# Performance work log

Hardware: AMD Instinct MI355X
Metric: run time of the kernel (lower is better)

Reference implementation:

```python
import jax, jax.numpy as jnp
import numpy as np

PAD_IND = 3
SOS_IND = 0
NSTEPS = 25
H = 256   # hidden_size
D = 256   # input_size (embedding dim)
L = 3     # lstm_layers


def _lstm_cell(x, h, c, Wih, Whh, bih, bhh):
    # torch LSTM gate order: i, f, g, o
    g = x @ Wih.T + bih + h @ Whh.T + bhh
    i, f, gg, o = jnp.split(g, 4, axis=-1)
    c2 = jax.nn.sigmoid(f) * c + jax.nn.sigmoid(i) * jnp.tanh(gg)
    h2 = jax.nn.sigmoid(o) * jnp.tanh(c2)
    return h2, c2


def setup_inputs() -> dict:
    key = jax.random.key(0)
    ks = jax.random.split(key, 24)
    B, T = 64, 256
    Vin, C = 32000, 32000
    s = 1.0 / np.sqrt(H)

    def u(k, shape):
        return jax.random.uniform(k, shape, jnp.float32, -s, s)

    return dict(
        x=jax.random.randint(ks[0], (B, T), 0, Vin),
        target_val=jax.random.randint(ks[1], (B, NSTEPS), 0, C),
        enc_embed=jax.random.normal(ks[2], (Vin, D), jnp.float32),
        enc_Wih=u(ks[3], (L, 4 * H, D)),
        enc_Whh=u(ks[4], (L, 4 * H, H)),
        enc_bih=u(ks[5], (L, 4 * H)),
        enc_bhh=u(ks[6], (L, 4 * H)),
        Wq=u(ks[7], (H, H)), bq=u(ks[8], (H,)),
        Wk=u(ks[9], (H, H)), bk=u(ks[10], (H,)),
        Wv=u(ks[11], (H, H)), bv=u(ks[12], (H,)),
        Wo=u(ks[13], (H, H)), bo=u(ks[14], (H,)),
        dec_embed=jax.random.normal(ks[15], (C, D), jnp.float32),
        dec_Wih0=u(ks[16], (4 * H, 2 * H)),            # decoder layer 0 input is [emb; ctx] = 2H
        dec_Wih_rest=u(ks[17], (L - 1, 4 * H, H)),
        dec_Whh=u(ks[18], (L, 4 * H, H)),
        dec_bih=u(ks[19], (L, 4 * H)),
        dec_bhh=u(ks[20], (L, 4 * H)),
        dec_W=u(ks[21], (C, H)),
        dec_b=u(ks[22], (C,)),
    )


def reference(x, target_val, enc_embed, enc_Wih, enc_Whh, enc_bih, enc_bhh,
              Wq, bq, Wk, bk, Wv, bv, Wo, bo,
              dec_embed, dec_Wih0, dec_Wih_rest, dec_Whh, dec_bih, dec_bhh,
              dec_W, dec_b):
    B, T = x.shape
    lengths = (x != PAD_IND).sum(axis=1)            # [B], emulates pack_padded_sequence
    emb = enc_embed[x]                              # [B,T,D]
    valid = (jnp.arange(T)[:, None] < lengths[None, :])[..., None]  # [T,B,1]
    h0 = jnp.zeros((L, B, H), emb.dtype)
    c0 = jnp.zeros((L, B, H), emb.dtype)

    def enc_step(carry, inp):
        h, c = carry
        xt, v = inp
        hs, cs = [], []
        z = xt
        for l in range(L):
            hl, cl = _lstm_cell(z, h[l], c[l], enc_Wih[l], enc_Whh[l], enc_bih[l], enc_bhh[l])
            hl = jnp.where(v, hl, h[l])             # freeze state past sequence length
            cl = jnp.where(v, cl, c[l])
            hs.append(hl); cs.append(cl)
            z = hl
        h = jnp.stack(hs); c = jnp.stack(cs)
        return (h, c), jnp.where(v, h[-1], 0.0)     # pad_packed pads with zeros

    (enc_h, enc_c), outs = jax.lax.scan(enc_step, (h0, c0), (jnp.swapaxes(emb, 0, 1), valid))
    enc_hiddens = jnp.swapaxes(outs, 0, 1)          # [B,T,H]

    # attention key/value projections are loop-invariant -> hoist out of decode loop
    kp = enc_hiddens @ Wk.T + bk                    # [B,T,H]
    vp = enc_hiddens @ Wv.T + bv                    # [B,T,H]
    scale = 1.0 / jnp.sqrt(jnp.asarray(H, emb.dtype))
    dec_Wih = [dec_Wih0, dec_Wih_rest[0], dec_Wih_rest[1]]
    tok0 = jnp.full((B,), SOS_IND, jnp.int32)

    def dec_step(carry, _):
        h, c, tok = carry
        e = dec_embed[tok]                          # [B,D]
        q = h.sum(axis=0) @ Wq.T + bq               # prev_state[0].sum(axis=0) -> [B,H]
        scores = jnp.einsum('bh,bth->bt', q, kp) * scale
        attn = jax.nn.softmax(scores, axis=-1)
        ctx = jnp.einsum('bt,bth->bh', attn, vp) @ Wo.T + bo
        z = jnp.concatenate([e, ctx], axis=-1)      # [B,2H]
        hs, cs = [], []
        for l in range(L):
            hl, cl = _lstm_cell(z, h[l], c[l], dec_Wih[l], dec_Whh[l], dec_bih[l], dec_bhh[l])
            hs.append(hl); cs.append(cl)
            z = hl
        h = jnp.stack(hs); c = jnp.stack(cs)
        logits = z @ dec_W.T + dec_b                # [B,C]
        tok = jnp.argmax(logits, axis=-1).astype(jnp.int32)  # greedy feedback (TF ratio = 0)
        return (h, c, tok), logits

    _, logits = jax.lax.scan(dec_step, (enc_h, enc_c, tok0), None, length=NSTEPS)  # [25,B,C]
    return jnp.swapaxes(logits, 0, 1)[:, :, None, :]  # [B,25,1,C] like the torch module
```

## Files before the change

kernel.cpp:

```cpp
#include <hip/hip_runtime.h>
#include <math.h>

#define TT    256
#define NB    64
#define HH    256
#define NSTEP 25
#define NCLS  32000
#define PADI  3

__device__ __align__(16) float g_hring[3][2][NB][HH];
__device__ __align__(16) float g_enchid[TT][NB][HH];
__device__ __align__(16) float g_kp[NB][TT][HH];
__device__ __align__(16) float g_vp[NB][TT][HH];
__device__ __align__(16) float g_cfin[3][NB][HH];
__device__ __align__(16) float g_hdec[2][3][NB][HH];
__device__ __align__(16) float g_z0[NB][512];
__device__ float    g_wmax[256][NB];
__device__ int      g_wmaxi[256][NB];
__device__ int      g_len[NB];
__device__ unsigned g_flags[256];

__global__ void k_zero_flags(){ g_flags[threadIdx.x] = 0u; }

__device__ __forceinline__ float sigf(float v){ return 1.0f / (1.0f + expf(-v)); }

#define SCOPE_AG __HIP_MEMORY_SCOPE_AGENT
typedef unsigned long long u64;
__device__ __forceinline__ float2 ld2(const float* p){
  u64 v = __hip_atomic_load((const u64*)p, __ATOMIC_RELAXED, SCOPE_AG);
  float2 r; __builtin_memcpy(&r, &v, 8); return r;
}
__device__ __forceinline__ void st2(float* p, float2 f){
  u64 v; __builtin_memcpy(&v, &f, 8);
  __hip_atomic_store((u64*)p, v, __ATOMIC_RELAXED, SCOPE_AG);
}
__device__ __forceinline__ float ldc(const float* p){ return __hip_atomic_load(p, __ATOMIC_RELAXED, SCOPE_AG); }
__device__ __forceinline__ void  stc(float* p, float v){ __hip_atomic_store(p, v, __ATOMIC_RELAXED, SCOPE_AG); }
__device__ __forceinline__ int   ldi(const int* p){ return __hip_atomic_load(p, __ATOMIC_RELAXED, SCOPE_AG); }
__device__ __forceinline__ void  sti(int* p, int v){ __hip_atomic_store(p, v, __ATOMIC_RELAXED, SCOPE_AG); }
__device__ __forceinline__ unsigned ldu(const unsigned* p){ return __hip_atomic_load(p, __ATOMIC_RELAXED, SCOPE_AG); }
__device__ __forceinline__ void  stu(unsigned* p, unsigned v){ __hip_atomic_store(p, v, __ATOMIC_RELAXED, SCOPE_AG); }

#define DOT4(a_, x_, w_) (a_) += (x_).x*(w_).x + (x_).y*(w_).y + (x_).z*(w_).z + (x_).w*(w_).w

#define WENC(cb,g,jj,u) (((((cb)*12+(g))*8+(jj))*36)+(u))

__device__ __forceinline__ void gbar(int w, unsigned target){
  asm volatile("s_waitcnt vmcnt(0)" ::: "memory");
  __syncthreads();
  if (threadIdx.x == 0) stu(&g_flags[w], target);
  if (threadIdx.x < 64){
    const int i4 = threadIdx.x * 4;
    for (;;){
      unsigned a0 = ldu(&g_flags[i4+0]);
      unsigned a1 = ldu(&g_flags[i4+1]);
      unsigned a2 = ldu(&g_flags[i4+2]);
      unsigned a3 = ldu(&g_flags[i4+3]);
      if (__all((a0>=target) && (a1>=target) && (a2>=target) && (a3>=target))) break;
      __builtin_amdgcn_s_sleep(1);
    }
  }
  __syncthreads();
}

template<int NCB, int BASE>
__device__ __forceinline__ void dec_gates(const float* sw, const float* i0, const float* i1,
                                          const float* i2, int j, float out4[4]){
  float a0=0.f, a1=0.f, a2=0.f, a3=0.f;
  const float* ips[3] = { i0, i1, i2 };
  #pragma unroll
  for (int cb = 0; cb < NCB; ++cb){
    float2 xin[16];
    #pragma unroll
    for (int u = 0; u < 16; ++u) xin[u] = ld2(ips[cb] + u*16 + 2*j);
    #pragma unroll
    for (int u2 = 0; u2 < 8; ++u2){
      float2 pa = xin[2*u2], pb = xin[2*u2+1];
      const float* wb = &sw[BASE + (((cb*4+0)*8+j)*36) + u2*4];
      float4 w0 = *(const float4*)(wb);
      float4 w1 = *(const float4*)(wb + 288);
      float4 w2 = *(const float4*)(wb + 576);
      float4 w3 = *(const float4*)(wb + 864);
      a0 += pa.x*w0.x + pa.y*w0.y + pb.x*w0.z + pb.y*w0.w;
      a1 += pa.x*w1.x + pa.y*w1.y + pb.x*w1.z + pb.y*w1.w;
      a2 += pa.x*w2.x + pa.y*w2.y + pb.x*w2.z + pb.y*w2.w;
      a3 += pa.x*w3.x + pa.y*w3.y + pb.x*w3.z + pb.y*w3.w;
    }
  }
  #pragma unroll
  for (int m = 1; m < 8; m <<= 1){
    a0 += __shfl_xor(a0, m); a1 += __shfl_xor(a1, m);
    a2 += __shfl_xor(a2, m); a3 += __shfl_xor(a3, m);
  }
  out4[0]=a0; out4[1]=a1; out4[2]=a2; out4[3]=a3;
}

__global__ void __launch_bounds__(512, 1)
k_main(const int*   __restrict__ p_x,
       const float* __restrict__ p_eemb,
       const float* __restrict__ p_eWih,  const float* __restrict__ p_eWhh,
       const float* __restrict__ p_ebih,  const float* __restrict__ p_ebhh,
       const float* __restrict__ p_Wq, const float* __restrict__ p_bq,
       const float* __restrict__ p_Wk, const float* __restrict__ p_bk,
       const float* __restrict__ p_Wv, const float* __restrict__ p_bv,
       const float* __restrict__ p_Wo, const float* __restrict__ p_bo,
       const float* __restrict__ p_demb,
       const float* __restrict__ p_dWih0, const float* __restrict__ p_dWihR,
       const float* __restrict__ p_dWhh,
       const float* __restrict__ p_dbih,  const float* __restrict__ p_dbhh,
       const float* __restrict__ p_dW,    const float* __restrict__ p_db,
       float* __restrict__ p_out)
{
  __shared__ __align__(16) float s_w[8064];
  __shared__ __align__(16) float s_h2[NB*HH];
  __shared__ float s_benc[12];
  __shared__ float s_bdec[12];
  __shared__ __align__(16) float s_hs[256];
  __shared__ __align__(16) float s_q[256];
  __shared__ __align__(16) float s_sc[256];
  __shared__ __align__(16) float s_at[256];
  __shared__ __align__(16) float s_ctx[256];
  __shared__ float s_rv[8];  __shared__ int s_ri[8];
  __shared__ float s_rv2[8][16]; __shared__ int s_ri2[8][16];

  const int w   = blockIdx.x;
  const int tid = threadIdx.x;
  const int b   = tid >> 3;
  const int j   = tid & 7;
  unsigned bar  = 0;

  const int lay0 = (w < 255) ? (w / 85) : 0;
  const int h0   = (w < 255) ? ((w - lay0*85) * 3) : 0;

  for (int fi = tid; fi < 6144; fi += 512){
    int g = fi >> 9, k = fi & 511;
    int e = g >> 2, gt = g & 3;
    int l   = (w < 255) ? lay0 : e;
    int hh2 = (w < 255) ? (h0 + e) : 255;
    int row = gt*256 + hh2;
    float v = (k < 256) ? p_eWih[((size_t)l*1024 + row)*256 + k]
                        : p_eWhh[((size_t)l*1024 + row)*256 + (k - 256)];
    int cb = k >> 8, kk = k & 255;
    s_w[WENC(cb, g, (kk & 15) >> 1, ((kk >> 4) << 1) | (kk & 1))] = v;
  }
  if (tid < 12){
    int e = tid >> 2, gt = tid & 3;
    int l   = (w < 255) ? lay0 : e;
    int hh2 = (w < 255) ? (h0 + e) : 255;
    int row = gt*256 + hh2;
    s_benc[tid] = p_ebih[l*1024 + row] + p_ebhh[l*1024 + row];
  }
  if (w < 64){
    int cnt = 0;
    if (tid < 256) cnt = (p_x[w*TT + tid] != PADI) ? 1 : 0;
    #pragma unroll
    for (int m = 1; m < 64; m <<= 1) cnt += __shfl_xor(cnt, m);
    if ((tid & 63) == 0) s_ri[tid >> 6] = cnt;
    __syncthreads();
    if (tid == 0){ int t2 = 0; for (int q2 = 0; q2 < 8; ++q2) t2 += s_ri[q2]; sti(&g_len[w], t2); }
  }
  if (tid < 192){
    int fi = w*192 + tid;
    int l = fi >> 14, rem = fi & 16383;
    stc(&g_hring[l][1][rem >> 8][rem & 255], 0.f);
  }
  gbar(w, ++bar);

  const int len_b = ldi(&g_len[b]);

  float c_reg[3] = {0.f,0.f,0.f};
  float h_reg[3] = {0.f,0.f,0.f};

  for (int sdiag = 0; sdiag < TT + 2; ++sdiag){
    float acc[12];
    #pragma unroll
    for (int g = 0; g < 12; ++g) acc[g] = 0.f;

    if (w < 255){
      const int t = sdiag - lay0;
      if (t >= 0 && t < TT){
        float2 x2[16], h2[16];
        if (lay0 == 0){
          const float* xs = p_eemb + (size_t)p_x[b*TT + t]*HH;
          #pragma unroll
          for (int u = 0; u < 16; ++u) x2[u] = *(const float2*)(xs + u*16 + 2*j);
        } else {
          const float* xs = &g_hring[lay0-1][t & 1][b][0];
          #pragma unroll
          for (int u = 0; u < 16; ++u) x2[u] = ld2(xs + u*16 + 2*j);
        }
        {
          const float* hsv = &g_hring[lay0][(t & 1) ^ 1][b][0];
          #pragma unroll
          for (int u = 0; u < 16; ++u) h2[u] = ld2(hsv + u*16 + 2*j);
        }
        #pragma unroll
        for (int u2 = 0; u2 < 8; ++u2){
          float2 xa = x2[2*u2], xb = x2[2*u2+1];
          float2 ha = h2[2*u2], hb = h2[2*u2+1];
          #pragma unroll
          for (int g = 0; g < 12; ++g){
            float4 wx = *(const float4*)&s_w[WENC(0, g, j, u2*4)];
            float4 wh = *(const float4*)&s_w[WENC(1, g, j, u2*4)];
            acc[g] += xa.x*wx.x + xa.y*wx.y + xb.x*wx.z + xb.y*wx.w
                    + ha.x*wh.x + ha.y*wh.y + hb.x*wh.z + hb.y*wh.w;
          }
        }
      }
    } else {
      #pragma unroll
      for (int e = 0; e < 3; ++e){
        const int t = sdiag - e;
        if (t >= 0 && t < TT){
          float2 x2[16], h2[16];
          if (e == 0){
            const float* xs = p_eemb + (size_t)p_x[b*TT + t]*HH;
            #pragma unroll
            for (int u = 0; u < 16; ++u) x2[u] = *(const float2*)(xs + u*16 + 2*j);
          } else {
            const float* xs = &g_hring[e-1][t & 1][b][0];
            #pragma unroll
            for (int u = 0; u < 16; ++u) x2[u] = ld2(xs + u*16 + 2*j);
          }
          {
            const float* hsv = &g_hring[e][(t & 1) ^ 1][b][0];
            #pragma unroll
            for (int u = 0; u < 16; ++u) h2[u] = ld2(hsv + u*16 + 2*j);
          }
          #pragma unroll
          for (int u2 = 0; u2 < 8; ++u2){
            float2 xa = x2[2*u2], xb = x2[2*u2+1];
            float2 ha = h2[2*u2], hb = h2[2*u2+1];
            #pragma unroll
            for (int g2 = 0; g2 < 4; ++g2){
              float4 wx = *(const float4*)&s_w[WENC(0, e*4+g2, j, u2*4)];
              float4 wh = *(const float4*)&s_w[WENC(1, e*4+g2, j, u2*4)];
              acc[e*4+g2] += xa.x*wx.x + xa.y*wx.y + xb.x*wx.z + xb.y*wx.w
                           + ha.x*wh.x + ha.y*wh.y + hb.x*wh.z + hb.y*wh.w;
            }
          }
        }
      }
    }

    #pragma unroll
    for (int g = 0; g < 12; ++g){
      float v = acc[g];
      v += __shfl_xor(v, 1); v += __shfl_xor(v, 2); v += __shfl_xor(v, 4);
      acc[g] = v;
    }

    if (j == 0){
      #pragma unroll
      for (int e = 0; e < 3; ++e){
        const int lay = (w < 255) ? lay0 : e;
        const int hh2 = (w < 255) ? (h0 + e) : 255;
        const int t = sdiag - lay;
        if (t >= 0 && t < TT){
          float iv = acc[e*4+0] + s_benc[e*4+0];
          float fv = acc[e*4+1] + s_benc[e*4+1];
          float gv = acc[e*4+2] + s_benc[e*4+2];
          float ov = acc[e*4+3] + s_benc[e*4+3];
          float c2 = sigf(fv)*c_reg[e] + sigf(iv)*tanhf(gv);
          float h2v = sigf(ov)*tanhf(c2);
          bool valid = (t < len_b);
          if (valid){ c_reg[e] = c2; h_reg[e] = h2v; }
          stc(&g_hring[lay][t & 1][b][hh2], h_reg[e]);
          if (lay == 2) stc(&g_enchid[t][b][hh2], valid ? h_reg[e] : 0.f);
        }
      }
    }
    gbar(w, ++bar);
  }

  if (j == 0){
    #pragma unroll
    for (int e = 0; e < 3; ++e){
      const int lay = (w < 255) ? lay0 : e;
      const int hh2 = (w < 255) ? (h0 + e) : 255;
      stc(&g_cfin[lay][b][hh2], c_reg[e]);
    }
  }
  gbar(w, ++bar);

  {
    const int b2 = w >> 2, t0 = (w & 3) * 64;
    const int n1 = tid & 127, rq = tid >> 7;
    for (int p = 0; p < 4; ++p){
      const int n = p*128 + n1;
      const float* wrow = (n < 256) ? (p_Wk + (size_t)n*HH) : (p_Wv + (size_t)(n-256)*HH);
      const float bias  = (n < 256) ? p_bk[n] : p_bv[n-256];
      const float4* wr4 = (const float4*)wrow;
      const float* hb = &g_enchid[t0 + rq*16][b2][0];
      const float4* hr[16];
      #pragma unroll
      for (int r = 0; r < 16; ++r) hr[r] = (const float4*)(hb + (size_t)r*NB*HH);
      float a16[16];
      #pragma unroll
      for (int r = 0; r < 16; ++r) a16[r] = 0.f;
      for (int k4 = 0; k4 < 64; ++k4){
        float4 wv = wr4[k4];
        #pragma unroll
        for (int r = 0; r < 16; ++r){ float4 h4 = hr[r][k4]; DOT4(a16[r], h4, wv); }
      }
      float* orow = (n < 256) ? &g_kp[b2][t0 + rq*16][n] : &g_vp[b2][t0 + rq*16][n-256];
      #pragma unroll
      for (int r = 0; r < 16; ++r) stc(orow + (size_t)r*HH, a16[r] + bias);
    }
  }

  for (int fi = tid; fi < 3072; fi += 512){
    int g = fi / 768, k = fi % 768; int row = g*256 + w;
    float v = (k < 512) ? p_dWih0[(size_t)row*512 + k]
                        : p_dWhh[(size_t)row*HH + (k - 512)];
    int cb = k >> 8, kk = k & 255;
    s_w[(((cb*4 + g)*8 + ((kk & 15) >> 1))*36) + (((kk >> 4) << 1) | (kk & 1))] = v;
  }
  for (int fi = tid; fi < 2048; fi += 512){
    int g = fi / 512, k = fi % 512; int row = g*256 + w;
    float v = (k < 256) ? p_dWihR[(size_t)row*HH + k]
                        : p_dWhh[(size_t)(1024 + row)*HH + (k - 256)];
    int cb = k >> 8, kk = k & 255;
    s_w[3456 + (((cb*4 + g)*8 + ((kk & 15) >> 1))*36) + (((kk >> 4) << 1) | (kk & 1))] = v;
  }
  for (int fi = tid; fi < 2048; fi += 512){
    int g = fi / 512, k = fi % 512; int row = g*256 + w;
    float v = (k < 256) ? p_dWihR[(size_t)(1024 + row)*HH + k]
                        : p_dWhh[(size_t)(2048 + row)*HH + (k - 256)];
    int cb = k >> 8, kk = k & 255;
    s_w[5760 + (((cb*4 + g)*8 + ((kk & 15) >> 1))*36) + (((kk >> 4) << 1) | (kk & 1))] = v;
  }
  if (tid < 12){
    int l = tid >> 2, g = tid & 3; int row = g*256 + w;
    s_bdec[tid] = p_dbih[l*1024 + row] + p_dbhh[l*1024 + row];
  }
  gbar(w, ++bar);

  if (tid < 192){
    int fi = w*192 + tid;
    int l = fi >> 14, rem = fi & 16383;
    stc(&g_hdec[0][l][rem >> 8][rem & 255], ldc(&g_hring[l][1][rem >> 8][rem & 255]));
  }
  float c_d0 = 0.f, c_d1 = 0.f, c_d2 = 0.f;
  if (j == 0){
    c_d0 = ldc(&g_cfin[0][b][w]); c_d1 = ldc(&g_cfin[1][b][w]); c_d2 = ldc(&g_cfin[2][b][w]);
  }
  gbar(w, ++bar);

  for (int st = 0; st < NSTEP; ++st){
    const int slot = st & 1, nxt = slot ^ 1;

    if (w < 64){
      const int bA = w;
      int tok = 0;
      if (st > 0){
        float v = -1e38f; int idx = 0;
        if (tid < 256){ v = ldc(&g_wmax[tid][bA]); idx = ldi(&g_wmaxi[tid][bA]); }
        #pragma unroll
        for (int m = 1; m < 64; m <<= 1){
          float ov = __shfl_xor(v, m); int oi = __shfl_xor(idx, m);
          if (ov > v || (ov == v && oi < idx)){ v = ov; idx = oi; }
        }
        if ((tid & 63) == 0){ s_rv[tid >> 6] = v; s_ri[tid >> 6] = idx; }
        __syncthreads();
        if (tid == 0){
          float bv2 = s_rv[0]; int bi2 = s_ri[0];
          for (int q2 = 1; q2 < 8; ++q2){
            float ov = s_rv[q2]; int oi = s_ri[q2];
            if (ov > bv2 || (ov == bv2 && oi < bi2)){ bv2 = ov; bi2 = oi; }
          }
          s_ri[0] = bi2;
        }
        __syncthreads();
        tok = s_ri[0];
      }
      if (tid < 256)
        s_hs[tid] = ldc(&g_hdec[slot][0][bA][tid]) + ldc(&g_hdec[slot][1][bA][tid])
                  + ldc(&g_hdec[slot][2][bA][tid]);
      __syncthreads();
      if (tid < 256){
        float a = p_bq[tid];
        const float4* wr = (const float4*)(p_Wq + (size_t)tid*HH);
        #pragma unroll 8
        for (int k4 = 0; k4 < 64; ++k4){
          float4 wv = wr[k4]; float4 h4 = *(const float4*)&s_hs[k4*4]; DOT4(a, h4, wv);
        }
        s_q[tid] = a;
      }
      __syncthreads();
      if (tid < 256){
        float a = 0.f;
        const float4* kr = (const float4*)&g_kp[bA][tid][0];
        #pragma unroll 8
        for (int k4 = 0; k4 < 64; ++k4){
          float4 kv = kr[k4]; float4 q4 = *(const float4*)&s_q[k4*4]; DOT4(a, q4, kv);
        }
        s_sc[tid] = a * 0.0625f;
      }
      __syncthreads();
      {
        float sv = (tid < 256) ? s_sc[tid] : -1e38f;
        float m2 = sv;
        #pragma unroll
        for (int m = 1; m < 64; m <<= 1) m2 = fmaxf(m2, __shfl_xor(m2, m));
        if ((tid & 63) == 0) s_rv[tid >> 6] = m2;
        __syncthreads();
        if (tid == 0){ float mm = s_rv[0]; for (int q2 = 1; q2 < 8; ++q2) mm = fmaxf(mm, s_rv[q2]); s_rv[0] = mm; }
        __syncthreads();
        const float mx = s_rv[0];
        float ev = (tid < 256) ? expf(sv - mx) : 0.f;
        float ss = ev;
        #pragma unroll
        for (int m = 1; m < 64; m <<= 1) ss += __shfl_xor(ss, m);
        __syncthreads();
        if ((tid & 63) == 0) s_rv[tid >> 6] = ss;
        __syncthreads();
        if (tid == 0){ float t2 = 0.f; for (int q2 = 0; q2 < 8; ++q2) t2 += s_rv[q2]; s_rv[0] = t2; }
        __syncthreads();
        if (tid < 256) s_at[tid] = ev / s_rv[0];
      }
      __syncthreads();
      if (tid < 256){
        float a = 0.f;
        const float* vb = &g_vp[bA][0][tid];
        #pragma unroll 4
        for (int t4 = 0; t4 < 64; ++t4){
          float4 a4 = *(const float4*)&s_at[t4*4];
          a += a4.x*vb[(size_t)(t4*4+0)*HH] + a4.y*vb[(size_t)(t4*4+1)*HH]
             + a4.z*vb[(size_t)(t4*4+2)*HH] + a4.w*vb[(size_t)(t4*4+3)*HH];
        }
        s_ctx[tid] = a;
      }
      __syncthreads();
      if (tid < 256){
        float a = p_bo[tid];
        const float4* wr = (const float4*)(p_Wo + (size_t)tid*HH);
        #pragma unroll 8
        for (int k4 = 0; k4 < 64; ++k4){
          float4 wv = wr[k4]; float4 c4 = *(const float4*)&s_ctx[k4*4]; DOT4(a, c4, wv);
        }
        stc(&g_z0[bA][256 + tid], a);
        stc(&g_z0[bA][tid], p_demb[(size_t)tok*HH + tid]);
      }
    }
    gbar(w, ++bar);

    {
      float g4[4];
      dec_gates<3, 0>(s_w, &g_z0[b][0], &g_z0[b][256], &g_hdec[slot][0][b][0], j, g4);
      if (j == 0){
        float iv = g4[0]+s_bdec[0], fv = g4[1]+s_bdec[1], gv = g4[2]+s_bdec[2], ov = g4[3]+s_bdec[3];
        float c2 = sigf(fv)*c_d0 + sigf(iv)*tanhf(gv); c_d0 = c2;
        stc(&g_hdec[nxt][0][b][w], sigf(ov)*tanhf(c2));
      }
    }
    gbar(w, ++bar);
    {
      float g4[4];
      dec_gates<2, 3456>(s_w, &g_hdec[nxt][0][b][0], &g_hdec[slot][1][b][0], nullptr, j, g4);
      if (j == 0){
        float iv = g4[0]+s_bdec[4], fv = g4[1]+s_bdec[5], gv = g4[2]+s_bdec[6], ov = g4[3]+s_bdec[7];
        float c2 = sigf(fv)*c_d1 + sigf(iv)*tanhf(gv); c_d1 = c2;
        stc(&g_hdec[nxt][1][b][w], sigf(ov)*tanhf(c2));
      }
    }
    gbar(w, ++bar);
    {
      float g4[4];
      dec_gates<2, 5760>(s_w, &g_hdec[nxt][1][b][0], &g_hdec[slot][2][b][0], nullptr, j, g4);
      if (j == 0){
        float iv = g4[0]+s_bdec[8], fv = g4[1]+s_bdec[9], gv = g4[2]+s_bdec[10], ov = g4[3]+s_bdec[11];
        float c2 = sigf(fv)*c_d2 + sigf(iv)*tanhf(gv); c_d2 = c2;
        stc(&g_hdec[nxt][2][b][w], sigf(ov)*tanhf(c2));
      }
    }
    gbar(w, ++bar);

    {
      {
        const float* src = &g_hdec[nxt][2][0][0];
        #pragma unroll
        for (int u = 0; u < 16; ++u){
          int fo = 2*(tid + 512*u);
          float2 v = ld2(src + fo);
          *(float2*)(s_h2 + fo) = v;
        }
      }
      __syncthreads();

      const int cq = tid & 127, qb = tid >> 7;
      const bool cok = (cq < 125);
      const int c  = w*125 + cq;
      const int cc = cok ? c : (w*125);
      const float4* wr = (const float4*)(p_dW + (size_t)cc*HH);
      const float4* zr[16];
      #pragma unroll
      for (int r = 0; r < 16; ++r) zr[r] = (const float4*)&s_h2[(qb*16 + r)*HH];
      float a16[16];
      #pragma unroll
      for (int r = 0; r < 16; ++r) a16[r] = 0.f;
      for (int k4 = 0; k4 < 64; ++k4){
        float4 wv = wr[k4];
        #pragma unroll
        for (int r = 0; r < 16; ++r){ float4 z4 = zr[r][k4]; DOT4(a16[r], z4, wv); }
      }
      const float bias = cok ? p_db[cc] : 0.f;
      #pragma unroll
      for (int r = 0; r < 16; ++r){
        const int bb = qb*16 + r;
        float val = a16[r] + bias;
        if (cok) p_out[((size_t)bb*NSTEP + st)*NCLS + c] = val;
        float v = cok ? val : -1e38f;
        int idx = cok ? c : 0x7fffffff;
        #pragma unroll
        for (int m = 1; m < 64; m <<= 1){
          float ov = __shfl_xor(v, m); int oi = __shfl_xor(idx, m);
          if (ov > v || (ov == v && oi < idx)){ v = ov; idx = oi; }
        }
        if ((tid & 63) == 0){ s_rv2[tid >> 6][r] = v; s_ri2[tid >> 6][r] = idx; }
      }
      __syncthreads();
      if (tid < 64){
        const int qb2 = tid >> 4, r = tid & 15;
        float v1 = s_rv2[qb2*2][r];   int i1 = s_ri2[qb2*2][r];
        float v2 = s_rv2[qb2*2+1][r]; int i2 = s_ri2[qb2*2+1][r];
        bool take2 = (v2 > v1) || (v2 == v1 && i2 < i1);
        stc(&g_wmax[w][qb2*16 + r],  take2 ? v2 : v1);
        sti(&g_wmaxi[w][qb2*16 + r], take2 ? i2 : i1);
      }
      __syncthreads();
    }
    gbar(w, ++bar);
  }
}

extern "C" void kernel_launch(void* const* d_in, const int* in_sizes, int n_in,
                              void* d_out, int out_size, void* d_ws, size_t ws_size,
                              hipStream_t stream){
  (void)in_sizes; (void)n_in; (void)out_size; (void)d_ws; (void)ws_size;
  const int*   x     = (const int*)d_in[0];
  const float* eemb  = (const float*)d_in[2];
  const float* eWih  = (const float*)d_in[3];
  const float* eWhh  = (const float*)d_in[4];
  const float* ebih  = (const float*)d_in[5];
  const float* ebhh  = (const float*)d_in[6];
  const float* Wq    = (const float*)d_in[7];
  const float* bq    = (const float*)d_in[8];
  const float* Wk    = (const float*)d_in[9];
  const float* bk    = (const float*)d_in[10];
  const float* Wv    = (const float*)d_in[11];
  const float* bv    = (const float*)d_in[12];
  const float* Wo    = (const float*)d_in[13];
  const float* bo    = (const float*)d_in[14];
  const float* demb  = (const float*)d_in[15];
  const float* dWih0 = (const float*)d_in[16];
  const float* dWihR = (const float*)d_in[17];
  const float* dWhh  = (const float*)d_in[18];
  const float* dbih  = (const float*)d_in[19];
  const float* dbhh  = (const float*)d_in[20];
  const float* dW    = (const float*)d_in[21];
  const float* db    = (const float*)d_in[22];
  float* out = (float*)d_out;

  k_zero_flags<<<dim3(1), dim3(256), 0, stream>>>();
  k_main<<<dim3(256), dim3(512), 0, stream>>>(
      x, eemb, eWih, eWhh, ebih, ebhh,
      Wq, bq, Wk, bk, Wv, bv, Wo, bo,
      demb, dWih0, dWihR, dWhh, dbih, dbhh, dW, db, out);
}
```

Baseline: 6.891 ms.

## Partition encoder by batch groups with per-group barriers and hierarchical grid barrier

The encoder wavefront is re-split so that each of four 64-block groups owns 16 batch rows for all three layers. Each block holds the weights for 12 hidden units (4 per layer) in shared memory and stages the group's hidden state into LDS once per diagonal step. This lets encoder steps synchronize only within a 64-block group instead of across the whole grid, and the full-grid barrier becomes a two-level flag scheme where one master block polls and then releases the rest. The cost is a larger LDS pool, repeated embedding gathers per block, and heavier per-step staging copies.

Result: slower. 7.721 ms (+12.1%).

```diff
diff --git a/kernel.cpp b/kernel.cpp
--- a/kernel.cpp
+++ b/kernel.cpp
@@ -18,9 +18,16 @@
 __device__ float    g_wmax[256][NB];
 __device__ int      g_wmaxi[256][NB];
 __device__ int      g_len[NB];
-__device__ unsigned g_flags[256];
-
-__global__ void k_zero_flags(){ g_flags[threadIdx.x] = 0u; }
+__device__ unsigned g_pa[256];
+__device__ unsigned g_pr[4];
+__device__ unsigned g_ga[256];
+__device__ unsigned g_gr;
+
+__global__ void k_zero_flags(){
+  g_pa[threadIdx.x] = 0u; g_ga[threadIdx.x] = 0u;
+  if (threadIdx.x < 4) g_pr[threadIdx.x] = 0u;
+  if (threadIdx.x == 0) g_gr = 0u;
+}
 
 __device__ __forceinline__ float sigf(float v){ return 1.0f / (1.0f + expf(-v)); }
 
@@ -29,10 +36,6 @@
 __device__ __forceinline__ float2 ld2(const float* p){
   u64 v = __hip_atomic_load((const u64*)p, __ATOMIC_RELAXED, SCOPE_AG);
   float2 r; __builtin_memcpy(&r, &v, 8); return r;
-}
-__device__ __forceinline__ void st2(float* p, float2 f){
-  u64 v; __builtin_memcpy(&v, &f, 8);
-  __hip_atomic_store((u64*)p, v, __ATOMIC_RELAXED, SCOPE_AG);
 }
 __device__ __forceinline__ float ldc(const float* p){ return __hip_atomic_load(p, __ATOMIC_RELAXED, SCOPE_AG); }
 __device__ __forceinline__ void  stc(float* p, float v){ __hip_atomic_store(p, v, __ATOMIC_RELAXED, SCOPE_AG); }
@@ -43,22 +46,45 @@
 
 #define DOT4(a_, x_, w_) (a_) += (x_).x*(w_).x + (x_).y*(w_).y + (x_).z*(w_).z + (x_).w*(w_).w
 
-#define WENC(cb,g,jj,u) (((((cb)*12+(g))*8+(jj))*36)+(u))
-
-__device__ __forceinline__ void gbar(int w, unsigned target){
+__device__ __forceinline__ void gbarP(int w, unsigned target){
   asm volatile("s_waitcnt vmcnt(0)" ::: "memory");
   __syncthreads();
-  if (threadIdx.x == 0) stu(&g_flags[w], target);
-  if (threadIdx.x < 64){
-    const int i4 = threadIdx.x * 4;
-    for (;;){
-      unsigned a0 = ldu(&g_flags[i4+0]);
-      unsigned a1 = ldu(&g_flags[i4+1]);
-      unsigned a2 = ldu(&g_flags[i4+2]);
-      unsigned a3 = ldu(&g_flags[i4+3]);
-      if (__all((a0>=target) && (a1>=target) && (a2>=target) && (a3>=target))) break;
-      __builtin_amdgcn_s_sleep(1);
-    }
+  const int grp = w >> 6, wl = w & 63;
+  if (threadIdx.x == 0) stu(&g_pa[w], target);
+  if (wl == 0){
+    if (threadIdx.x < 64){
+      for (;;){
+        unsigned a = ldu(&g_pa[(grp << 6) + threadIdx.x]);
+        if (__all(a >= target)) break;
+        __builtin_amdgcn_s_sleep(1);
+      }
+      if (threadIdx.x == 0) stu(&g_pr[grp], target);
+    }
+  } else if (threadIdx.x == 0){
+    while (ldu(&g_pr[grp]) < target) __builtin_amdgcn_s_sleep(1);
+  }
+  __syncthreads();
+}
+
+__device__ __forceinline__ void gbarG(int w, unsigned target){
+  asm volatile("s_waitcnt vmcnt(0)" ::: "memory");
+  __syncthreads();
+  if (threadIdx.x == 0) stu(&g_ga[w], target);
+  if (w == 0){
+    if (threadIdx.x < 64){
+      const int i4 = threadIdx.x * 4;
+      for (;;){
+        unsigned a0 = ldu(&g_ga[i4+0]);
+        unsigned a1 = ldu(&g_ga[i4+1]);
+        unsigned a2 = ldu(&g_ga[i4+2]);
+        unsigned a3 = ldu(&g_ga[i4+3]);
+        if (__all((a0>=target) && (a1>=target) && (a2>=target) && (a3>=target))) break;
+        __builtin_amdgcn_s_sleep(1);
+      }
+      if (threadIdx.x == 0) stu(&g_gr, target);
+    }
+  } else if (threadIdx.x == 0){
+    while (ldu(&g_gr) < target) __builtin_amdgcn_s_sleep(1);
   }
   __syncthreads();
 }
@@ -94,6 +120,8 @@
   }
   out4[0]=a0; out4[1]=a1; out4[2]=a2; out4[3]=a3;
 }
+
+#define POOL_FL 38080
 
 __global__ void __launch_bounds__(512, 1)
 k_main(const int*   __restrict__ p_x,
@@ -111,45 +139,53 @@
        const float* __restrict__ p_dW,    const float* __restrict__ p_db,
        float* __restrict__ p_out)
 {
-  __shared__ __align__(16) float s_w[8064];
-  __shared__ __align__(16) float s_h2[NB*HH];
-  __shared__ float s_benc[12];
-  __shared__ float s_bdec[12];
+  __shared__ __align__(16) float s_pool[POOL_FL];
+  __shared__ int   s_len[16];
   __shared__ __align__(16) float s_hs[256];
   __shared__ __align__(16) float s_q[256];
   __shared__ __align__(16) float s_sc[256];
   __shared__ __align__(16) float s_at[256];
   __shared__ __align__(16) float s_ctx[256];
+  __shared__ float s_bdec[12];
   __shared__ float s_rv[8];  __shared__ int s_ri[8];
   __shared__ float s_rv2[8][16]; __shared__ int s_ri2[8][16];
 
+  float* const s_W     = s_pool;
+  float* const s_stage = s_pool + 24576;
+  float* const s_gat   = s_pool + 36864;
+  float* const s_c     = s_pool + 37632;
+  float* const s_hfrz  = s_pool + 37824;
+  float* const s_bias  = s_pool + 38016;
+
   const int w   = blockIdx.x;
   const int tid = threadIdx.x;
-  const int b   = tid >> 3;
-  const int j   = tid & 7;
-  unsigned bar  = 0;
-
-  const int lay0 = (w < 255) ? (w / 85) : 0;
-  const int h0   = (w < 255) ? ((w - lay0*85) * 3) : 0;
-
-  for (int fi = tid; fi < 6144; fi += 512){
-    int g = fi >> 9, k = fi & 511;
-    int e = g >> 2, gt = g & 3;
-    int l   = (w < 255) ? lay0 : e;
-    int hh2 = (w < 255) ? (h0 + e) : 255;
-    int row = gt*256 + hh2;
-    float v = (k < 256) ? p_eWih[((size_t)l*1024 + row)*256 + k]
-                        : p_eWhh[((size_t)l*1024 + row)*256 + (k - 256)];
-    int cb = k >> 8, kk = k & 255;
-    s_w[WENC(cb, g, (kk & 15) >> 1, ((kk >> 4) << 1) | (kk & 1))] = v;
-  }
-  if (tid < 12){
-    int e = tid >> 2, gt = tid & 3;
-    int l   = (w < 255) ? lay0 : e;
-    int hh2 = (w < 255) ? (h0 + e) : 255;
-    int row = gt*256 + hh2;
-    s_benc[tid] = p_ebih[l*1024 + row] + p_ebhh[l*1024 + row];
-  }
+  unsigned barP = 0, barG = 0;
+
+  const int grp = w >> 6, wl = w & 63;
+  const int gb0 = grp << 4;
+  const int bg = tid >> 7;
+  const int sg = (tid >> 4) & 7;
+  const int jk = tid & 15;
+  const int b  = tid >> 3;
+  const int j  = tid & 7;
+
+  for (int fi = tid; fi < 24576; fi += 512){
+    int row = fi >> 9, k = fi & 511;
+    int su = row >> 2, gate = row & 3;
+    int lay = su >> 2;
+    int hh  = (wl + (su << 6)) & 255;
+    int wrow = gate*256 + hh;
+    s_W[fi] = (k < 256) ? p_eWih[((size_t)lay*1024 + wrow)*256 + k]
+                        : p_eWhh[((size_t)lay*1024 + wrow)*256 + (k - 256)];
+  }
+  if (tid < 48){
+    int su = tid >> 2, gate = tid & 3;
+    int lay = su >> 2;
+    int hh  = (wl + (su << 6)) & 255;
+    int wrow = gate*256 + hh;
+    s_bias[tid] = p_ebih[lay*1024 + wrow] + p_ebhh[lay*1024 + wrow];
+  }
+  if (tid < 192){ s_c[tid] = 0.f; s_hfrz[tid] = 0.f; }
   if (w < 64){
     int cnt = 0;
     if (tid < 256) cnt = (p_x[w*TT + tid] != PADI) ? 1 : 0;
@@ -159,139 +195,125 @@
     __syncthreads();
     if (tid == 0){ int t2 = 0; for (int q2 = 0; q2 < 8; ++q2) t2 += s_ri[q2]; sti(&g_len[w], t2); }
   }
+  if (tid < 384){
+    int fi = w*384 + tid;
+    stc(&((float*)g_hring)[fi], 0.f);
+  }
+  gbarG(w, ++barG);
+
+  if (tid < 16) s_len[tid] = ldi(&g_len[gb0 + tid]);
+
+  for (int d = 0; d < TT + 2; ++d){
+    {
+      const float* b0 = &g_hring[0][(d-1)&1][gb0][0];
+      const float* b1 = &g_hring[1][ d   &1][gb0][0];
+      const float* b2 = &g_hring[2][(d-1)&1][gb0][0];
+      #pragma unroll
+      for (int m = 0; m < 12; ++m){
+        const float* src = ((m < 4) ? b0 : (m < 8) ? b1 : b2) + (m & 3)*1024 + tid*2;
+        float2 v = ld2(src);
+        *(float2*)&s_stage[m*1024 + tid*2] = v;
+      }
+    }
+    __syncthreads();
+
+    const int t0c = (d < TT) ? d : (TT - 1);
+    int tok[4];
+    #pragma unroll
+    for (int bb = 0; bb < 4; ++bb) tok[bb] = p_x[(gb0 + bg*4 + bb)*TT + t0c];
+
+    float acc[6][4];
+    #pragma unroll
+    for (int m = 0; m < 6; ++m){ acc[m][0]=0.f; acc[m][1]=0.f; acc[m][2]=0.f; acc[m][3]=0.f; }
+
+    #pragma unroll
+    for (int kc = 0; kc < 4; ++kc){
+      const int ko = kc*64 + jk*4;
+      float4 e4[4], h0v[4], h1v[4], h2v[4];
+      #pragma unroll
+      for (int bb = 0; bb < 4; ++bb){
+        const int lb = bg*4 + bb;
+        e4[bb]  = *(const float4*)(p_eemb + (size_t)tok[bb]*HH + ko);
+        h0v[bb] = *(const float4*)&s_stage[        lb*256 + ko];
+        h1v[bb] = *(const float4*)&s_stage[4096  + lb*256 + ko];
+        h2v[bb] = *(const float4*)&s_stage[8192  + lb*256 + ko];
+      }
+      #pragma unroll
+      for (int m = 0; m < 6; ++m){
+        const int row = sg + 8*m;
+        float4 wx = *(const float4*)&s_W[row*512 + ko];
+        float4 wh = *(const float4*)&s_W[row*512 + 256 + ko];
+        #pragma unroll
+        for (int bb = 0; bb < 4; ++bb){
+          float4 xs = (m < 2) ? e4[bb]  : (m < 4) ? h0v[bb] : h1v[bb];
+          float4 hs = (m < 2) ? h0v[bb] : (m < 4) ? h1v[bb] : h2v[bb];
+          acc[m][bb] += xs.x*wx.x + xs.y*wx.y + xs.z*wx.z + xs.w*wx.w
+                      + hs.x*wh.x + hs.y*wh.y + hs.z*wh.z + hs.w*wh.w;
+        }
+      }
+    }
+
+    #pragma unroll
+    for (int m = 0; m < 6; ++m){
+      #pragma unroll
+      for (int bb = 0; bb < 4; ++bb){
+        float v = acc[m][bb];
+        v += __shfl_xor(v, 1); v += __shfl_xor(v, 2);
+        v += __shfl_xor(v, 4); v += __shfl_xor(v, 8);
+        acc[m][bb] = v;
+      }
+    }
+    if (jk == 0){
+      #pragma unroll
+      for (int m = 0; m < 6; ++m){
+        #pragma unroll
+        for (int bb = 0; bb < 4; ++bb)
+          s_gat[(sg + 8*m)*16 + bg*4 + bb] = acc[m][bb];
+      }
+    }
+    __syncthreads();
+
+    if (tid < 192){
+      const int su = tid >> 4, lb = tid & 15;
+      const int lay = su >> 2;
+      const int hh  = (wl + (su << 6)) & 255;
+      const int t = d - lay;
+      if (t >= 0 && t < TT){
+        float iv = s_gat[(su*4+0)*16 + lb] + s_bias[su*4+0];
+        float fv = s_gat[(su*4+1)*16 + lb] + s_bias[su*4+1];
+        float gv = s_gat[(su*4+2)*16 + lb] + s_bias[su*4+2];
+        float ov = s_gat[(su*4+3)*16 + lb] + s_bias[su*4+3];
+        float cc = s_c[tid], hp = s_hfrz[tid];
+        float c2 = sigf(fv)*cc + sigf(iv)*tanhf(gv);
+        float h2x = sigf(ov)*tanhf(c2);
+        bool valid = (t < s_len[lb]);
+        float ho = valid ? h2x : hp;
+        if (valid) s_c[tid] = c2;
+        s_hfrz[tid] = ho;
+        stc(&g_hring[lay][t & 1][gb0 + lb][hh], ho);
+        if (lay == 2) stc(&g_enchid[t][gb0 + lb][hh], valid ? ho : 0.f);
+      }
+    }
+    gbarP(w, ++barP);
+  }
+
   if (tid < 192){
-    int fi = w*192 + tid;
-    int l = fi >> 14, rem = fi & 16383;
-    stc(&g_hring[l][1][rem >> 8][rem & 255], 0.f);
-  }
-  gbar(w, ++bar);
-
-  const int len_b = ldi(&g_len[b]);
-
-  float c_reg[3] = {0.f,0.f,0.f};
-  float h_reg[3] = {0.f,0.f,0.f};
-
-  for (int sdiag = 0; sdiag < TT + 2; ++sdiag){
-    float acc[12];
-    #pragma unroll
-    for (int g = 0; g < 12; ++g) acc[g] = 0.f;
-
-    if (w < 255){
-      const int t = sdiag - lay0;
-      if (t >= 0 && t < TT){
-        float2 x2[16], h2[16];
-        if (lay0 == 0){
-          const float* xs = p_eemb + (size_t)p_x[b*TT + t]*HH;
-          #pragma unroll
-          for (int u = 0; u < 16; ++u) x2[u] = *(const float2*)(xs + u*16 + 2*j);
-        } else {
-          const float* xs = &g_hring[lay0-1][t & 1][b][0];
-          #pragma unroll
-          for (int u = 0; u < 16; ++u) x2[u] = ld2(xs + u*16 + 2*j);
-        }
-        {
-          const float* hsv = &g_hring[lay0][(t & 1) ^ 1][b][0];
-          #pragma unroll
-          for (int u = 0; u < 16; ++u) h2[u] = ld2(hsv + u*16 + 2*j);
-        }
-        #pragma unroll
-        for (int u2 = 0; u2 < 8; ++u2){
-          float2 xa = x2[2*u2], xb = x2[2*u2+1];
-          float2 ha = h2[2*u2], hb = h2[2*u2+1];
-          #pragma unroll
-          for (int g = 0; g < 12; ++g){
-            float4 wx = *(const float4*)&s_w[WENC(0, g, j, u2*4)];
-            float4 wh = *(const float4*)&s_w[WENC(1, g, j, u2*4)];
-            acc[g] += xa.x*wx.x + xa.y*wx.y + xb.x*wx.z + xb.y*wx.w
-                    + ha.x*wh.x + ha.y*wh.y + hb.x*wh.z + hb.y*wh.w;
-          }
-        }
-      }
-    } else {
-      #pragma unroll
-      for (int e = 0; e < 3; ++e){
-        const int t = sdiag - e;
-        if (t >= 0 && t < TT){
-          float2 x2[16], h2[16];
-          if (e == 0){
-            const float* xs = p_eemb + (size_t)p_x[b*TT + t]*HH;
-            #pragma unroll
-            for (int u = 0; u < 16; ++u) x2[u] = *(const float2*)(xs + u*16 + 2*j);
-          } else {
-            const float* xs = &g_hring[e-1][t & 1][b][0];
-            #pragma unroll
-            for (int u = 0; u < 16; ++u) x2[u] = ld2(xs + u*16 + 2*j);
-          }
-          {
-            const float* hsv = &g_hring[e][(t & 1) ^ 1][b][0];
-            #pragma unroll
-            for (int u = 0; u < 16; ++u) h2[u] = ld2(hsv + u*16 + 2*j);
-          }
-          #pragma unroll
-          for (int u2 = 0; u2 < 8; ++u2){
-            float2 xa = x2[2*u2], xb = x2[2*u2+1];
-            float2 ha = h2[2*u2], hb = h2[2*u2+1];
-            #pragma unroll
-            for (int g2 = 0; g2 < 4; ++g2){
-              float4 wx = *(const float4*)&s_w[WENC(0, e*4+g2, j, u2*4)];
-              float4 wh = *(const float4*)&s_w[WENC(1, e*4+g2, j, u2*4)];
-              acc[e*4+g2] += xa.x*wx.x + xa.y*wx.y + xb.x*wx.z + xb.y*wx.w
-                           + ha.x*wh.x + ha.y*wh.y + hb.x*wh.z + hb.y*wh.w;
-            }
-          }
-        }
-      }
-    }
-
-    #pragma unroll
-    for (int g = 0; g < 12; ++g){
-      float v = acc[g];
-      v += __shfl_xor(v, 1); v += __shfl_xor(v, 2); v += __shfl_xor(v, 4);
-      acc[g] = v;
-    }
-
-    if (j == 0){
-      #pragma unroll
-      for (int e = 0; e < 3; ++e){
-        const int lay = (w < 255) ? lay0 : e;
-        const int hh2 = (w < 255) ? (h0 + e) : 255;
-        const int t = sdiag - lay;
-        if (t >= 0 && t < TT){
-          float iv = acc[e*4+0] + s_benc[e*4+0];
-          float fv = acc[e*4+1] + s_benc[e*4+1];
-          float gv = acc[e*4+2] + s_benc[e*4+2];
-          float ov = acc[e*4+3] + s_benc[e*4+3];
-          float c2 = sigf(fv)*c_reg[e] + sigf(iv)*tanhf(gv);
-          float h2v = sigf(ov)*tanhf(c2);
-          bool valid = (t < len_b);
-          if (valid){ c_reg[e] = c2; h_reg[e] = h2v; }
-          stc(&g_hring[lay][t & 1][b][hh2], h_reg[e]);
-          if (lay == 2) stc(&g_enchid[t][b][hh2], valid ? h_reg[e] : 0.f);
-        }
-      }
-    }
-    gbar(w, ++bar);
-  }
-
-  if (j == 0){
-    #pragma unroll
-    for (int e = 0; e < 3; ++e){
-      const int lay = (w < 255) ? lay0 : e;
-      const int hh2 = (w < 255) ? (h0 + e) : 255;
-      stc(&g_cfin[lay][b][hh2], c_reg[e]);
-    }
-  }
-  gbar(w, ++bar);
+    const int su = tid >> 4, lb = tid & 15;
+    const int lay = su >> 2;
+    const int hh  = (wl + (su << 6)) & 255;
+    stc(&g_cfin[lay][gb0 + lb][hh], s_c[tid]);
+  }
+  gbarG(w, ++barG);
 
   {
-    const int b2 = w >> 2, t0 = (w & 3) * 64;
+    const int b3 = w >> 2, t0 = (w & 3) * 64;
     const int n1 = tid & 127, rq = tid >> 7;
     for (int p = 0; p < 4; ++p){
       const int n = p*128 + n1;
       const float* wrow = (n < 256) ? (p_Wk + (size_t)n*HH) : (p_Wv + (size_t)(n-256)*HH);
       const float bias  = (n < 256) ? p_bk[n] : p_bv[n-256];
       const float4* wr4 = (const float4*)wrow;
-      const float* hb = &g_enchid[t0 + rq*16][b2][0];
+      const float* hb = &g_enchid[t0 + rq*16][b3][0];
       const float4* hr[16];
       #pragma unroll
       for (int r = 0; r < 16; ++r) hr[r] = (const float4*)(hb + (size_t)r*NB*HH);
@@ -303,38 +325,41 @@
         #pragma unroll
         for (int r = 0; r < 16; ++r){ float4 h4 = hr[r][k4]; DOT4(a16[r], h4, wv); }
       }
-      float* orow = (n < 256) ? &g_kp[b2][t0 + rq*16][n] : &g_vp[b2][t0 + rq*16][n-256];
+      float* orow = (n < 256) ? &g_kp[b3][t0 + rq*16][n] : &g_vp[b3][t0 + rq*16][n-256];
       #pragma unroll
       for (int r = 0; r < 16; ++r) stc(orow + (size_t)r*HH, a16[r] + bias);
     }
   }
 
-  for (int fi = tid; fi < 3072; fi += 512){
-    int g = fi / 768, k = fi % 768; int row = g*256 + w;
-    float v = (k < 512) ? p_dWih0[(size_t)row*512 + k]
-                        : p_dWhh[(size_t)row*HH + (k - 512)];
-    int cb = k >> 8, kk = k & 255;
-    s_w[(((cb*4 + g)*8 + ((kk & 15) >> 1))*36) + (((kk >> 4) << 1) | (kk & 1))] = v;
-  }
-  for (int fi = tid; fi < 2048; fi += 512){
-    int g = fi / 512, k = fi % 512; int row = g*256 + w;
-    float v = (k < 256) ? p_dWihR[(size_t)row*HH + k]
-                        : p_dWhh[(size_t)(1024 + row)*HH + (k - 256)];
-    int cb = k >> 8, kk = k & 255;
-    s_w[3456 + (((cb*4 + g)*8 + ((kk & 15) >> 1))*36) + (((kk >> 4) << 1) | (kk & 1))] = v;
-  }
-  for (int fi = tid; fi < 2048; fi += 512){
-    int g = fi / 512, k = fi % 512; int row = g*256 + w;
-    float v = (k < 256) ? p_dWihR[(size_t)(1024 + row)*HH + k]
-                        : p_dWhh[(size_t)(2048 + row)*HH + (k - 256)];
-    int cb = k >> 8, kk = k & 255;
-    s_w[5760 + (((cb*4 + g)*8 + ((kk & 15) >> 1))*36) + (((kk >> 4) << 1) | (kk & 1))] = v;
-  }
-  if (tid < 12){
-    int l = tid >> 2, g = tid & 3; int row = g*256 + w;
-    s_bdec[tid] = p_dbih[l*1024 + row] + p_dbhh[l*1024 + row];
-  }
-  gbar(w, ++bar);
+  {
+    float* s_w = s_pool;
+    for (int fi = tid; fi < 3072; fi += 512){
+      int g = fi / 768, k = fi % 768; int row = g*256 + w;
+      float v = (k < 512) ? p_dWih0[(size_t)row*512 + k]
+                          : p_dWhh[(size_t)row*HH + (k - 512)];
+      int cb = k >> 8, kk = k & 255;
+      s_w[(((cb*4 + g)*8 + ((kk & 15) >> 1))*36) + (((kk >> 4) << 1) | (kk & 1))] = v;
+    }
+    for (int fi = tid; fi < 2048; fi += 512){
+      int g = fi / 512, k = fi % 512; int row = g*256 + w;
+      float v = (k < 256) ? p_dWihR[(size_t)row*HH + k]
+                          : p_dWhh[(size_t)(1024 + row)*HH + (k - 256)];
+      int cb = k >> 8, kk = k & 255;
+      s_w[3456 + (((cb*4 + g)*8 + ((kk & 15) >> 1))*36) + (((kk >> 4) << 1) | (kk & 1))] = v;
+    }
+    for (int fi = tid; fi < 2048; fi += 512){
+      int g = fi / 512, k = fi % 512; int row = g*256 + w;
+      float v = (k < 256) ? p_dWihR[(size_t)(1024 + row)*HH + k]
+                          : p_dWhh[(size_t)(2048 + row)*HH + (k - 256)];
+      int cb = k >> 8, kk = k & 255;
+      s_w[5760 + (((cb*4 + g)*8 + ((kk & 15) >> 1))*36) + (((kk >> 4) << 1) | (kk & 1))] = v;
+    }
+    if (tid < 12){
+      int l = tid >> 2, g = tid & 3; int row = g*256 + w;
+      s_bdec[tid] = p_dbih[l*1024 + row] + p_dbhh[l*1024 + row];
+    }
+  }
+  gbarG(w, ++barG);
 
   if (tid < 192){
     int fi = w*192 + tid;
@@ -345,7 +370,10 @@
   if (j == 0){
     c_d0 = ldc(&g_cfin[0][b][w]); c_d1 = ldc(&g_cfin[1][b][w]); c_d2 = ldc(&g_cfin[2][b][w]);
   }
-  gbar(w, ++bar);
+  gbarG(w, ++barG);
+
+  float* const s_w  = s_pool;
+  float* const s_h2 = s_pool + 8064;
 
   for (int st = 0; st < NSTEP; ++st){
     const int slot = st & 1, nxt = slot ^ 1;
@@ -443,7 +471,7 @@
         stc(&g_z0[bA][tid], p_demb[(size_t)tok*HH + tid]);
       }
     }
-    gbar(w, ++bar);
+    gbarG(w, ++barG);
 
     {
       float g4[4];
@@ -454,7 +482,7 @@
         stc(&g_hdec[nxt][0][b][w], sigf(ov)*tanhf(c2));
       }
     }
-    gbar(w, ++bar);
+    gbarG(w, ++barG);
     {
       float g4[4];
       dec_gates<2, 3456>(s_w, &g_hdec[nxt][0][b][0], &g_hdec[slot][1][b][0], nullptr, j, g4);
@@ -464,7 +492,7 @@
         stc(&g_hdec[nxt][1][b][w], sigf(ov)*tanhf(c2));
       }
     }
-    gbar(w, ++bar);
+    gbarG(w, ++barG);
     {
       float g4[4];
       dec_gates<2, 5760>(s_w, &g_hdec[nxt][1][b][0], &g_hdec[slot][2][b][0], nullptr, j, g4);
@@ -474,7 +502,7 @@
         stc(&g_hdec[nxt][2][b][w], sigf(ov)*tanhf(c2));
       }
     }
-    gbar(w, ++bar);
+    gbarG(w, ++barG);
 
     {
       {
@@ -530,7 +558,7 @@
       }
       __syncthreads();
     }
-    gbar(w, ++bar);
+    gbarG(w, ++barG);
   }
 }
 
```
